# Performance work log

Measured on AMD Instinct MI355X. Metric: run time of the kernel, lower is better.

Reference implementation:

```python
import jax, jax.numpy as jnp
import numpy as np

NODE_DIM = 128
HIDDEN = 64
N_NODES = 2048


def setup_inputs() -> dict:
    key = jax.random.key(0)
    ks = jax.random.split(key, 7)
    s_enc = 1.0 / np.sqrt(NODE_DIM)
    s1 = 1.0 / np.sqrt(2 * HIDDEN)
    s2 = 1.0 / np.sqrt(HIDDEN)
    return {
        "node_features": jax.random.normal(ks[0], (N_NODES, NODE_DIM), dtype=jnp.float32),
        "W_enc": jax.random.uniform(ks[1], (NODE_DIM, HIDDEN), jnp.float32, -s_enc, s_enc),
        "b_enc": jax.random.uniform(ks[2], (HIDDEN,), jnp.float32, -s_enc, s_enc),
        "W1": jax.random.uniform(ks[3], (2 * HIDDEN, HIDDEN), jnp.float32, -s1, s1),
        "b1": jax.random.uniform(ks[4], (HIDDEN,), jnp.float32, -s1, s1),
        "W2": jax.random.uniform(ks[5], (HIDDEN, 1), jnp.float32, -s2, s2),
        "b2": jax.random.uniform(ks[6], (1,), jnp.float32, -s2, s2),
    }


def reference(node_features, W_enc, b_enc, W1, b1, W2, b2):
    # node encoder: (n, node_dim) -> (n, hidden)
    h = node_features @ W_enc + b_enc
    # split first edge-MLP weight into the halves acting on h_i and h_j of the concat
    Wa, Wb = W1[:HIDDEN], W1[HIDDEN:]
    a = h @ Wa  # (n, hidden) contribution from source node i
    b = h @ Wb  # (n, hidden) contribution from target node j
    # pairwise pre-activation: (n, n, hidden) == Linear(concat(h_i, h_j))
    z = jax.nn.relu(a[:, None, :] + b[None, :, :] + b1)
    logits = jnp.einsum("ijh,ho->ijo", z, W2)[..., 0] + b2[0]  # (n, n)
    T = jax.nn.sigmoid(logits)
    # diagonal is never written in the original loop -> stays 0
    n = T.shape[0]
    return T * (1.0 - jnp.eye(n, dtype=T.dtype))
```

## Files before the change

### kernel.cpp

```cpp
#include <hip/hip_runtime.h>
#include <math.h>

#define NODE_DIM 128
#define HIDDEN   64
#define NN       2048
#define LSTR     68

typedef float v4f __attribute__((ext_vector_type(4)));

__global__ __launch_bounds__(256) void prep_kernel(
    const float* __restrict__ nf, const float* __restrict__ W_enc,
    const float* __restrict__ b_enc, const float* __restrict__ W1,
    const float* __restrict__ b1, const float* __restrict__ W2,
    float* __restrict__ A, float* __restrict__ BB,
    float* __restrict__ pa, float* __restrict__ pb)
{
    __shared__ float nf_s[4][NODE_DIM];
    __shared__ float h_s[4][HIDDEN];
    __shared__ float ra_s[4][HIDDEN];
    __shared__ float rb_s[4][HIDDEN];
    const int tid = threadIdx.x;
    const int rg  = tid >> 6;
    const int t   = tid & 63;
    const int r   = blockIdx.x * 4 + rg;

    ((float2*)nf_s[rg])[t] = ((const float2*)(nf + (size_t)r * NODE_DIM))[t];
    __syncthreads();

    float acc = b_enc[t];
    #pragma unroll 8
    for (int k = 0; k < NODE_DIM; ++k)
        acc = fmaf(nf_s[rg][k], W_enc[k * HIDDEN + t], acc);
    h_s[rg][t] = acc;
    __syncthreads();

    float aacc = 0.0f;
    float bacc = b1[t];
    #pragma unroll 8
    for (int k = 0; k < HIDDEN; ++k) {
        const float hv = h_s[rg][k];
        aacc = fmaf(hv, W1[k * HIDDEN + t], aacc);
        bacc = fmaf(hv, W1[(HIDDEN + k) * HIDDEN + t], bacc);
    }
    A[(size_t)r * HIDDEN + t]  = aacc;
    BB[(size_t)r * HIDDEN + t] = bacc;

    const float wv = W2[t];
    ra_s[rg][t] = wv * aacc;
    rb_s[rg][t] = wv * bacc;
    __syncthreads();

    #pragma unroll
    for (int s = 32; s > 0; s >>= 1) {
        if (t < s) {
            ra_s[rg][t] += ra_s[rg][t + s];
            rb_s[rg][t] += rb_s[rg][t + s];
        }
        __syncthreads();
    }
    if (t == 0) { pa[r] = ra_s[rg][0]; pb[r] = rb_s[rg][0]; }
}

__global__ __launch_bounds__(256, 1) void pair_kernel(
    const float* __restrict__ A, const float* __restrict__ BB,
    const float* __restrict__ pa, const float* __restrict__ pb,
    const float* __restrict__ W2, const float* __restrict__ b2,
    float* __restrict__ out)
{
    __shared__ __align__(16) float aL[128 * LSTR];
    __shared__ __align__(16) float bL[128 * LSTR];

    const int tid = threadIdx.x;
    const int i0  = blockIdx.y * 128;
    const int j0  = blockIdx.x * 128;

    const v4f* gA = (const v4f*)(A  + (size_t)i0 * HIDDEN);
    const v4f* gB = (const v4f*)(BB + (size_t)j0 * HIDDEN);
    #pragma unroll
    for (int k = 0; k < 8; ++k) {
        const int idx = tid + k * 256;
        const int row = idx >> 4;
        const int c   = idx & 15;
        *(v4f*)&aL[row * LSTR + c * 4] = gA[idx];
        *(v4f*)&bL[row * LSTR + c * 4] = gB[idx];
    }
    __syncthreads();

    const int ty = tid >> 4;
    const int tx = tid & 15;

    float acc[8][8] = {{0.0f}};

    #pragma unroll 2
    for (int c = 0; c < 16; ++c) {
        const float w0 = W2[c * 4 + 0];
        const float w1 = W2[c * 4 + 1];
        const float w2 = W2[c * 4 + 2];
        const float w3 = W2[c * 4 + 3];
        v4f av[8], bv[8];
        #pragma unroll
        for (int ii = 0; ii < 8; ++ii)
            av[ii] = *(const v4f*)&aL[(ty + 16 * ii) * LSTR + c * 4];
        #pragma unroll
        for (int jj = 0; jj < 8; ++jj)
            bv[jj] = *(const v4f*)&bL[(tx + 16 * jj) * LSTR + c * 4];
        #pragma unroll
        for (int ii = 0; ii < 8; ++ii) {
            #pragma unroll
            for (int jj = 0; jj < 8; ++jj) {
                const v4f t = av[ii] + bv[jj];
                float s = acc[ii][jj];
                s = fmaf(__builtin_fabsf(t[0]), w0, s);
                s = fmaf(__builtin_fabsf(t[1]), w1, s);
                s = fmaf(__builtin_fabsf(t[2]), w2, s);
                s = fmaf(__builtin_fabsf(t[3]), w3, s);
                acc[ii][jj] = s;
            }
        }
    }

    const float b2v = b2[0];
    float par[8], pbr[8];
    #pragma unroll
    for (int ii = 0; ii < 8; ++ii) par[ii] = pa[i0 + ty + 16 * ii];
    #pragma unroll
    for (int jj = 0; jj < 8; ++jj) pbr[jj] = pb[j0 + tx + 16 * jj];

    #pragma unroll
    for (int ii = 0; ii < 8; ++ii) {
        const int i = i0 + ty + 16 * ii;
        #pragma unroll
        for (int jj = 0; jj < 8; ++jj) {
            const int j = j0 + tx + 16 * jj;
            const float lg = fmaf(0.5f, par[ii] + pbr[jj] + acc[ii][jj], b2v);
            const float sg = 1.0f / (1.0f + __expf(-lg));
            out[(size_t)i * NN + j] = (i == j) ? 0.0f : sg;
        }
    }
}

extern "C" void kernel_launch(void* const* d_in, const int* in_sizes, int n_in,
                              void* d_out, int out_size, void* d_ws, size_t ws_size,
                              hipStream_t stream) {
    const float* nf    = (const float*)d_in[0];
    const float* W_enc = (const float*)d_in[1];
    const float* b_enc = (const float*)d_in[2];
    const float* W1    = (const float*)d_in[3];
    const float* b1    = (const float*)d_in[4];
    const float* W2    = (const float*)d_in[5];
    const float* b2    = (const float*)d_in[6];
    float* out = (float*)d_out;

    float* A  = (float*)d_ws;
    float* BB = A + (size_t)NN * HIDDEN;
    float* pa = BB + (size_t)NN * HIDDEN;
    float* pb = pa + NN;

    prep_kernel<<<NN / 4, 256, 0, stream>>>(nf, W_enc, b_enc, W1, b1, W2,
                                            A, BB, pa, pb);
    pair_kernel<<<dim3(NN / 128, NN / 128), 256, 0, stream>>>(
        A, BB, pa, pb, W2, b2, out);
}
```

Before: 102.8 us.

## Split hidden-dimension reduction across two thread halves in pair kernel

```diff
diff --git a/kernel.cpp b/kernel.cpp
--- a/kernel.cpp
+++ b/kernel.cpp
@@ -61,14 +61,15 @@
     if (t == 0) { pa[r] = ra_s[rg][0]; pb[r] = rb_s[rg][0]; }
 }
 
-__global__ __launch_bounds__(256, 1) void pair_kernel(
+__global__ __launch_bounds__(512, 2) void pair_kernel(
     const float* __restrict__ A, const float* __restrict__ BB,
     const float* __restrict__ pa, const float* __restrict__ pb,
     const float* __restrict__ W2, const float* __restrict__ b2,
     float* __restrict__ out)
 {
-    __shared__ __align__(16) float aL[128 * LSTR];
-    __shared__ __align__(16) float bL[128 * LSTR];
+    __shared__ __align__(16) float smem[2 * 128 * LSTR];
+    float* aL = smem;
+    float* bL = smem + 128 * LSTR;
 
     const int tid = threadIdx.x;
     const int i0  = blockIdx.y * 128;
@@ -77,8 +78,8 @@
     const v4f* gA = (const v4f*)(A  + (size_t)i0 * HIDDEN);
     const v4f* gB = (const v4f*)(BB + (size_t)j0 * HIDDEN);
     #pragma unroll
-    for (int k = 0; k < 8; ++k) {
-        const int idx = tid + k * 256;
+    for (int k = 0; k < 4; ++k) {
+        const int idx = tid + k * 512;
         const int row = idx >> 4;
         const int c   = idx & 15;
         *(v4f*)&aL[row * LSTR + c * 4] = gA[idx];
@@ -86,13 +87,17 @@
     }
     __syncthreads();
 
-    const int ty = tid >> 4;
-    const int tx = tid & 15;
+    const int half = tid >> 8;
+    const int t    = tid & 255;
+    const int ty   = t >> 4;
+    const int tx   = t & 15;
+    const int hb   = half * 8;
 
     float acc[8][8] = {{0.0f}};
 
     #pragma unroll 2
-    for (int c = 0; c < 16; ++c) {
+    for (int cc = 0; cc < 8; ++cc) {
+        const int c = hb + cc;
         const float w0 = W2[c * 4 + 0];
         const float w1 = W2[c * 4 + 1];
         const float w2 = W2[c * 4 + 2];
@@ -108,31 +113,55 @@
         for (int ii = 0; ii < 8; ++ii) {
             #pragma unroll
             for (int jj = 0; jj < 8; ++jj) {
-                const v4f t = av[ii] + bv[jj];
+                const v4f tv = av[ii] + bv[jj];
                 float s = acc[ii][jj];
-                s = fmaf(__builtin_fabsf(t[0]), w0, s);
-                s = fmaf(__builtin_fabsf(t[1]), w1, s);
-                s = fmaf(__builtin_fabsf(t[2]), w2, s);
-                s = fmaf(__builtin_fabsf(t[3]), w3, s);
+                s = fmaf(__builtin_fabsf(tv[0]), w0, s);
+                s = fmaf(__builtin_fabsf(tv[1]), w1, s);
+                s = fmaf(__builtin_fabsf(tv[2]), w2, s);
+                s = fmaf(__builtin_fabsf(tv[3]), w3, s);
                 acc[ii][jj] = s;
             }
         }
     }
 
+    __syncthreads();
+    float* cbuf = smem;
+
+    if (half == 0) {
+        #pragma unroll
+        for (int s = 0; s < 32; ++s) {
+            const int slot = 32 + s;
+            cbuf[slot * 256 + t] = acc[slot >> 3][slot & 7];
+        }
+    } else {
+        #pragma unroll
+        for (int s = 0; s < 32; ++s) {
+            cbuf[s * 256 + t] = acc[s >> 3][s & 7];
+        }
+    }
+    __syncthreads();
+
     const float b2v = b2[0];
-    float par[8], pbr[8];
-    #pragma unroll
-    for (int ii = 0; ii < 8; ++ii) par[ii] = pa[i0 + ty + 16 * ii];
-    #pragma unroll
-    for (int jj = 0; jj < 8; ++jj) pbr[jj] = pb[j0 + tx + 16 * jj];
-
-    #pragma unroll
-    for (int ii = 0; ii < 8; ++ii) {
-        const int i = i0 + ty + 16 * ii;
+    if (half == 0) {
         #pragma unroll
-        for (int jj = 0; jj < 8; ++jj) {
+        for (int s = 0; s < 32; ++s) {
+            const int ii = s >> 3, jj = s & 7;
+            const int i = i0 + ty + 16 * ii;
             const int j = j0 + tx + 16 * jj;
-            const float lg = fmaf(0.5f, par[ii] + pbr[jj] + acc[ii][jj], b2v);
+            const float S = acc[ii][jj] + cbuf[s * 256 + t];
+            const float lg = fmaf(0.5f, pa[i] + pb[j] + S, b2v);
+            const float sg = 1.0f / (1.0f + __expf(-lg));
+            out[(size_t)i * NN + j] = (i == j) ? 0.0f : sg;
+        }
+    } else {
+        #pragma unroll
+        for (int s = 0; s < 32; ++s) {
+            const int slot = 32 + s;
+            const int ii = slot >> 3, jj = slot & 7;
+            const int i = i0 + ty + 16 * ii;
+            const int j = j0 + tx + 16 * jj;
+            const float S = acc[ii][jj] + cbuf[slot * 256 + t];
+            const float lg = fmaf(0.5f, pa[i] + pb[j] + S, b2v);
             const float sg = 1.0f / (1.0f + __expf(-lg));
             out[(size_t)i * NN + j] = (i == j) ? 0.0f : sg;
         }
@@ -158,6 +187,6 @@
 
     prep_kernel<<<NN / 4, 256, 0, stream>>>(nf, W_enc, b_enc, W1, b1, W2,
                                             A, BB, pa, pb);
-    pair_kernel<<<dim3(NN / 128, NN / 128), 256, 0, stream>>>(
+    pair_kernel<<<dim3(NN / 128, NN / 128), 512, 0, stream>>>(
         A, BB, pa, pb, W2, b2, out);
 }
```

Result: faster. 100.4 us (-2.3%).
